# Performance work log

Measured on AMD Instinct MI355X. Metric: run time of the kernel, lower is better.

## Reference

```python
import jax, jax.numpy as jnp
import numpy as np

# dims: batch, nodes, d_node, d_edge, d_attn_hid, heads, d_node_hid, d_edge_hid, layers
B, N, DN, DE, DH, H, DNH, DEH, L = 2, 256, 128, 64, 128, 8, 512, 256, 2
DHH = DH // H  # per-head dim
SCALE = 1.0 / (DH ** 0.5)  # source scales by full d_hid, not per-head dim


def _ln(x, g, b):
    m = jnp.mean(x, -1, keepdims=True)
    v = jnp.mean((x - m) ** 2, -1, keepdims=True)
    return (x - m) * jax.lax.rsqrt(v + 1e-5) * g + b


def _gelu(x):
    return jax.nn.gelu(x, approximate=False)  # torch nn.GELU default = exact erf


def setup_inputs() -> dict:
    key = jax.random.key(0)
    ks = iter(jax.random.split(key, 40))
    def w(shape, scale=0.02):
        return jax.random.normal(next(ks), shape, jnp.float32) * scale
    return {
        "node_features": jax.random.normal(next(ks), (B, N, DN), jnp.float32),
        "edge_features": jax.random.normal(next(ks), (B, N, N, DE), jnp.float32),
        "Wqkv_n": w((L, DN, 3 * DH)),
        "Wqkv_e": w((L, DE, 4 * DH)),
        "Wo": w((L, DH, DN)), "bo": jnp.zeros((L, DN), jnp.float32),
        "Wl0": w((L, DN, DN)), "bl0": jnp.zeros((L, DN), jnp.float32),
        "ln0_g": jnp.ones((L, DN), jnp.float32), "ln0_b": jnp.zeros((L, DN), jnp.float32),
        "Wm1": w((L, DN, DNH)), "Wm2": w((L, DNH, DN)), "bm2": jnp.zeros((L, DN), jnp.float32),
        "ln1_g": jnp.ones((L, DN), jnp.float32), "ln1_b": jnp.zeros((L, DN), jnp.float32),
        "We0": w((L, 2 * DE, DEH)), "be0": jnp.zeros((L, DEH), jnp.float32),
        "Ws": w((L, DN, DEH)), "bs": jnp.zeros((L, DEH), jnp.float32),
        "Wt": w((L, DN, DEH)), "bt": jnp.zeros((L, DEH), jnp.float32),
        "We1": w((L, DEH, DE)), "be1": jnp.zeros((L, DE), jnp.float32),
        "eln0_g": jnp.ones((L, DE), jnp.float32), "eln0_b": jnp.zeros((L, DE), jnp.float32),
        "Wem1": w((L, DE, DEH)), "Wem2": w((L, DEH, DE)), "bem2": jnp.zeros((L, DE), jnp.float32),
        "eln1_g": jnp.ones((L, DE), jnp.float32), "eln1_b": jnp.zeros((L, DE), jnp.float32),
    }


def _forward(node_features, edge_features, Wqkv_n, Wqkv_e, Wo, bo, Wl0, bl0,
             ln0_g, ln0_b, Wm1, Wm2, bm2, ln1_g, ln1_b, We0, be0, Ws, bs, Wt, bt,
             We1, be1, eln0_g, eln0_b, Wem1, Wem2, bem2, eln1_g, eln1_b):
    x, e = node_features, edge_features
    for l in range(L):
        # --- RTAttention (modulate_v=True, eval mode) ---
        qkv_n = (x @ Wqkv_n[l]).reshape(B, N, H, 3 * DHH).transpose(0, 2, 1, 3)  # b h n 3d
        qn, kn, vn = jnp.split(qkv_n, 3, axis=-1)
        qkv_e = (e @ Wqkv_e[l]).reshape(B, N, N, H, 4 * DHH).transpose(0, 3, 1, 2, 4)  # b h i j 4d
        eq, ek, ev, em = jnp.split(qkv_e, 4, axis=-1)
        q = qn[:, :, :, None, :] + eq            # b h i j d
        k = kn[:, :, None, :, :] + ek            # b h i j d
        v = vn[:, :, None, :, :] * em + ev       # modulated values
        dots = SCALE * jnp.einsum('bhijd,bhijd->bhij', q, k)
        attn = jax.nn.softmax(dots, axis=-1)
        out = jnp.einsum('bhij,bhijd->bhid', attn, v)
        out = out.transpose(0, 2, 1, 3).reshape(B, N, DH)
        attn_out = out @ Wo[l] + bo[l]
        # --- node updates: ln(x + lin0(attn)); ln(x + mlp(x)) ---
        x = _ln(x + (attn_out @ Wl0[l] + bl0[l]), ln0_g[l], ln0_b[l])
        x = _ln(x + (_gelu(x @ Wm1[l]) @ Wm2[l] + bm2[l]), ln1_g[l], ln1_b[l])
        # --- edge updates (EdgeLayer) ---
        src = (x @ Ws[l] + bs[l])[:, :, None, :]   # broadcast over target j
        tgt = (x @ Wt[l] + bt[l])[:, None, :, :]   # broadcast over source i
        ecat = jnp.concatenate([e, e.transpose(0, 2, 1, 3)], axis=-1)  # [e_ij, e_ji]
        h = _gelu(ecat @ We0[l] + be0[l] + src + tgt)
        e = _ln(e + (h @ We1[l] + be1[l]), eln0_g[l], eln0_b[l])
        e = _ln(e + (_gelu(e @ Wem1[l]) @ Wem2[l] + bem2[l]), eln1_g[l], eln1_b[l])
    return x, e


def reference(node_features, edge_features, Wqkv_n, Wqkv_e, Wo, bo, Wl0, bl0,
              ln0_g, ln0_b, Wm1, Wm2, bm2, ln1_g, ln1_b, We0, be0, Ws, bs, Wt, bt,
              We1, be1, eln0_g, eln0_b, Wem1, Wem2, bem2, eln1_g, eln1_b):
    return _forward(node_features, edge_features, Wqkv_n, Wqkv_e, Wo, bo, Wl0, bl0,
                    ln0_g, ln0_b, Wm1, Wm2, bm2, ln1_g, ln1_b, We0, be0, Ws, bs, Wt, bt,
                    We1, be1, eln0_g, eln0_b, Wem1, Wem2, bem2, eln1_g, eln1_b)
```

## Files before the change

### kernel.cpp

```cpp
#include <hip/hip_runtime.h>
#include <hip/hip_bf16.h>
#include <stdint.h>

#define BB 2
#define NN 256
#define DN 128
#define DE 64
#define DH 128
#define NH 8
#define DHH 16
#define DNH 512
#define DEH 256
#define NL 2
#define SCALE_ATT 0.08838834764831845f

typedef __hip_bfloat16 bf16;
typedef __attribute__((ext_vector_type(8))) short short8;
typedef __attribute__((ext_vector_type(4))) float f32x4;

__device__ __forceinline__ float gelu_f(float x) {
  return 0.5f * x * (1.0f + erff(x * 0.70710678118654752f));
}
__device__ __forceinline__ float gelu_t(float x) {
  float m2u = x * fmaf(x * x, -0.07135481627f, -1.59576912161f);
  float e = __expf(m2u);
  return x * __builtin_amdgcn_rcpf(1.f + e);
}

template <int ctrl>
__device__ __forceinline__ float dppf(float v) {
  return __int_as_float(
      __builtin_amdgcn_update_dpp(0, __float_as_int(v), ctrl, 0xF, 0xF, true));
}
__device__ __forceinline__ float row_sum16(float v) {
  v += dppf<0xB1>(v);
  v += dppf<0x4E>(v);
  v += dppf<0x124>(v);
  v += dppf<0x128>(v);
  return v;
}
__device__ __forceinline__ float row_max16(float v) {
  v = fmaxf(v, dppf<0xB1>(v));
  v = fmaxf(v, dppf<0x4E>(v));
  v = fmaxf(v, dppf<0x124>(v));
  v = fmaxf(v, dppf<0x128>(v));
  return v;
}
__device__ __forceinline__ float wave_sum(float v) {
  v = row_sum16(v);
  v += __shfl_xor(v, 16, 64);
  v += __shfl_xor(v, 32, 64);
  return v;
}
__device__ __forceinline__ float wave_max(float v) {
  v = row_max16(v);
  v = fmaxf(v, __shfl_xor(v, 16, 64));
  v = fmaxf(v, __shfl_xor(v, 32, 64));
  return v;
}

__device__ __forceinline__ short f2bf(float f) {
  union { float f; uint32_t u; } v{f};
  uint32_t r = (v.u + 0x7FFFu + ((v.u >> 16) & 1u)) >> 16;
  return (short)r;
}
__device__ __forceinline__ float bf2f(short s) {
  union { uint32_t u; float f; } v;
  v.u = ((uint32_t)(uint16_t)s) << 16;
  return v.f;
}

__global__ void k_detect(const uint32_t* g8, const uint32_t* g13, int* flag) {
  if (threadIdx.x == 0 && blockIdx.x == 0) {
    uint32_t a = g8[0], b = g13[0];
    *flag = (a == 0x3F803F80u || b == 0x3F803F80u) ? 1 : 0;
  }
}

struct CastArgs {
  const void* src[30];
  float* dst[30];
  int n[30];
  const int* flag;
};

__global__ __launch_bounds__(256) void k_cast_all(CastArgs a) {
  int ti = blockIdx.y;
  float* d = a.dst[ti];
  int n = a.n[ti];
  int stride = gridDim.x * blockDim.x;
  if (*a.flag) {
    const bf16* s = (const bf16*)a.src[ti];
    for (int i = blockIdx.x * blockDim.x + threadIdx.x; i < n; i += stride)
      d[i] = __bfloat162float(s[i]);
  } else {
    const float* s = (const float*)a.src[ti];
    for (int i = blockIdx.x * blockDim.x + threadIdx.x; i < n; i += stride)
      d[i] = s[i];
  }
}

__global__ __launch_bounds__(256) void k_cast_e(const void* __restrict__ src,
                                                short* __restrict__ dst,
                                                const int* __restrict__ flag) {
  const int n8 = BB * NN * NN * DE / 8;
  int stride = gridDim.x * blockDim.x;
  if (*flag) {
    const uint4* s = (const uint4*)src;
    uint4* d = (uint4*)dst;
    for (int i = blockIdx.x * blockDim.x + threadIdx.x; i < n8; i += stride) d[i] = s[i];
  } else {
    const float4* s = (const float4*)src;
    for (int i = blockIdx.x * blockDim.x + threadIdx.x; i < n8; i += stride) {
      float4 a = s[2 * i], b = s[2 * i + 1];
      short* o = dst + 8 * i;
      o[0] = f2bf(a.x); o[1] = f2bf(a.y); o[2] = f2bf(a.z); o[3] = f2bf(a.w);
      o[4] = f2bf(b.x); o[5] = f2bf(b.y); o[6] = f2bf(b.z); o[7] = f2bf(b.w);
    }
  }
}

__global__ __launch_bounds__(256) void k_cast_out(const float* __restrict__ x,
                                                  const short* __restrict__ e,
                                                  void* __restrict__ out_v,
                                                  const int* __restrict__ flag) {
  const int nx = BB * NN * DN;
  const int total = nx + BB * NN * NN * DE;
  int stride = gridDim.x * blockDim.x;
  if (*flag) {
    short* out = (short*)out_v;
    for (int i = blockIdx.x * blockDim.x + threadIdx.x; i < total; i += stride)
      out[i] = (i < nx) ? f2bf(x[i]) : e[i - nx];
  } else {
    float* out = (float*)out_v;
    for (int i = blockIdx.x * blockDim.x + threadIdx.x; i < total; i += stride)
      out[i] = (i < nx) ? x[i] : bf2f(e[i - nx]);
  }
}

struct WtJob { const float* src; short* dst; int K; int N; };
struct WtArgs { WtJob job[10]; };
__global__ __launch_bounds__(256) void k_wtrans_all(WtArgs a) {
  WtJob j = a.job[blockIdx.y];
  int total = j.K * j.N;
  int stride = gridDim.x * 256;
  for (int idx = blockIdx.x * 256 + threadIdx.x; idx < total; idx += stride) {
    int k = idx / j.N, n = idx - k * j.N;
    j.dst[n * j.K + k] = f2bf(j.src[idx]);
  }
}

__global__ __launch_bounds__(128) void k_node_qkv(const float* __restrict__ x,
                                                  const float* __restrict__ W,
                                                  float* __restrict__ qkv) {
  int row = blockIdx.x;
  __shared__ float xs[DN];
  int t = threadIdx.x;
  xs[t] = x[row * DN + t];
  __syncthreads();
#pragma unroll
  for (int c0 = 0; c0 < 384; c0 += 128) {
    int c = c0 + t;
    float a = 0.f;
    for (int k = 0; k < DN; ++k) a = fmaf(xs[k], W[k * 384 + c], a);
    qkv[row * 384 + c] = a;
  }
}

__global__ __launch_bounds__(256) void k_attn_fused(
    const short* __restrict__ e, const short* __restrict__ WqeT,
    const float* __restrict__ qkv, float* __restrict__ o_buf) {
  int i = blockIdx.x, b = blockIdx.y;
  __shared__ short est[256 * 72];
  __shared__ float sp[NH * NN];
  __shared__ float qnl[DH];
  int t = threadIdx.x;
  for (int idx = t; idx < 2048; idx += 256) {
    int j = idx >> 3, c8 = (idx & 7) * 8;
    *(short8*)(est + j * 72 + c8) =
        *(const short8*)(e + ((size_t)(b * NN + i) * NN + j) * DE + c8);
  }
  if (t < DH) qnl[t] = qkv[(size_t)(b * NN + i) * 384 + (t >> 4) * 48 + (t & 15)];
  __syncthreads();

  int wv = t >> 6, lane = t & 63, g8 = lane >> 4, lo = lane & 15;

  {
    short8 bq[2][2][2];
#pragma unroll
    for (int hh = 0; hh < 2; ++hh)
#pragma unroll
      for (int p = 0; p < 2; ++p)
#pragma unroll
        for (int ks = 0; ks < 2; ++ks)
          bq[hh][p][ks] = *(const short8*)(
              WqeT + (size_t)(((wv * 2 + hh) * 4 + p) * 16 + lo) * 64 + ks * 32 + g8 * 8);
    for (int mt = 0; mt < 16; ++mt) {
      short8 a0 = *(const short8*)(est + (mt * 16 + lo) * 72 + g8 * 8);
      short8 a1 = *(const short8*)(est + (mt * 16 + lo) * 72 + 32 + g8 * 8);
#pragma unroll
      for (int hh = 0; hh < 2; ++hh) {
        int h = wv * 2 + hh;
        float kn4[4];
#pragma unroll
        for (int r = 0; r < 4; ++r)
          kn4[r] = qkv[(size_t)(b * NN + mt * 16 + g8 * 4 + r) * 384 + h * 48 + 16 + lo];
        f32x4 cq = {0.f, 0.f, 0.f, 0.f}, ck = {0.f, 0.f, 0.f, 0.f};
        cq = __builtin_amdgcn_mfma_f32_16x16x32_bf16(a0, bq[hh][0][0], cq, 0, 0, 0);
        cq = __builtin_amdgcn_mfma_f32_16x16x32_bf16(a1, bq[hh][0][1], cq, 0, 0, 0);
        ck = __builtin_amdgcn_mfma_f32_16x16x32_bf16(a0, bq[hh][1][0], ck, 0, 0, 0);
        ck = __builtin_amdgcn_mfma_f32_16x16x32_bf16(a1, bq[hh][1][1], ck, 0, 0, 0);
        float qv = qnl[h * 16 + lo];
#pragma unroll
        for (int r = 0; r < 4; ++r) {
          int j = mt * 16 + g8 * 4 + r;
          float s = (qv + cq[r]) * (kn4[r] + ck[r]);
          s = row_sum16(s);
          if (lo == 0) sp[h * NN + j] = s * SCALE_ATT;
        }
      }
    }
  }
  __syncthreads();

#pragma unroll
  for (int hh = 0; hh < 2; ++hh) {
    int h = wv * 2 + hh;
    float v[4];
#pragma unroll
    for (int q = 0; q < 4; ++q) v[q] = sp[h * NN + lane + 64 * q];
    float m = fmaxf(fmaxf(v[0], v[1]), fmaxf(v[2], v[3]));
    m = wave_max(m);
    float l = 0.f;
#pragma unroll
    for (int q = 0; q < 4; ++q) { v[q] = __expf(v[q] - m); l += v[q]; }
    l = wave_sum(l);
    float inv = 1.f / l;
#pragma unroll
    for (int q = 0; q < 4; ++q) sp[h * NN + lane + 64 * q] = v[q] * inv;
  }
  __syncthreads();

  {
    short8 bv[2][2][2];
#pragma unroll
    for (int hh = 0; hh < 2; ++hh)
#pragma unroll
      for (int p = 0; p < 2; ++p)
#pragma unroll
        for (int ks = 0; ks < 2; ++ks)
          bv[hh][p][ks] = *(const short8*)(
              WqeT + (size_t)(((wv * 2 + hh) * 4 + 2 + p) * 16 + lo) * 64 + ks * 32 + g8 * 8);
    float oacc[2] = {0.f, 0.f};
    for (int mt = 0; mt < 16; ++mt) {
      short8 a0 = *(const short8*)(est + (mt * 16 + lo) * 72 + g8 * 8);
      short8 a1 = *(const short8*)(est + (mt * 16 + lo) * 72 + 32 + g8 * 8);
#pragma unroll
      for (int hh = 0; hh < 2; ++hh) {
        int h = wv * 2 + hh;
        float vn4[4];
#pragma unroll
        for (int r = 0; r < 4; ++r)
          vn4[r] = qkv[(size_t)(b * NN + mt * 16 + g8 * 4 + r) * 384 + h * 48 + 32 + lo];
        f32x4 cv = {0.f, 0.f, 0.f, 0.f}, cm = {0.f, 0.f, 0.f, 0.f};
        cv = __builtin_amdgcn_mfma_f32_16x16x32_bf16(a0, bv[hh][0][0], cv, 0, 0, 0);
        cv = __builtin_amdgcn_mfma_f32_16x16x32_bf16(a1, bv[hh][0][1], cv, 0, 0, 0);
        cm = __builtin_amdgcn_mfma_f32_16x16x32_bf16(a0, bv[hh][1][0], cm, 0, 0, 0);
        cm = __builtin_amdgcn_mfma_f32_16x16x32_bf16(a1, bv[hh][1][1], cm, 0, 0, 0);
#pragma unroll
        for (int r = 0; r < 4; ++r) {
          int j = mt * 16 + g8 * 4 + r;
          float vv = fmaf(vn4[r], cm[r], cv[r]);
          oacc[hh] = fmaf(sp[h * NN + j], vv, oacc[hh]);
        }
      }
    }
#pragma unroll
    for (int hh = 0; hh < 2; ++hh) {
      int h = wv * 2 + hh;
      float o = oacc[hh];
      o += __shfl_xor(o, 16, 64);
      o += __shfl_xor(o, 32, 64);
      if (g8 == 0) o_buf[(size_t)(b * NN + i) * DH + h * 16 + lo] = o;
    }
  }
}

__global__ __launch_bounds__(256) void k_node_fused(
    const float* __restrict__ o_buf,
    const float* __restrict__ Wo, const float* __restrict__ bo,
    const float* __restrict__ Wl0, const float* __restrict__ bl0,
    const float* __restrict__ g0, const float* __restrict__ b0n,
    const float* __restrict__ Wm1, const float* __restrict__ Wm2,
    const float* __restrict__ bm2, const float* __restrict__ g1,
    const float* __restrict__ b1n, const float* __restrict__ Ws,
    const float* __restrict__ bs, const float* __restrict__ Wt,
    const float* __restrict__ bt, const float* __restrict__ WqnN,
    float* __restrict__ qkv, float* __restrict__ srcb,
    float* __restrict__ tgtb, float* __restrict__ x) {
  int i = blockIdx.x, b = blockIdx.y;
  int row = b * NN + i;
  __shared__ float orow[DH];
  __shared__ float t1s[DH];
  __shared__ float xs[DN];
  __shared__ float hsb[DNH];
  __shared__ float part[256];
  __shared__ float red[4];
  int t = threadIdx.x;
  int col = t & 127, kh = t >> 7;
  if (t < DH) orow[t] = o_buf[(size_t)row * DH + t];
  __syncthreads();
  {
    float a = 0.f;
    int k0 = kh * 64;
    for (int k = k0; k < k0 + 64; ++k) a = fmaf(orow[k], Wo[k * DN + col], a);
    part[t] = a;
  }
  __syncthreads();
  if (t < DH) t1s[t] = part[t] + part[t + 128] + bo[t];
  __syncthreads();
  {
    float a = 0.f;
    int k0 = kh * 64;
    for (int k = k0; k < k0 + 64; ++k) a = fmaf(t1s[k], Wl0[k * DN + col], a);
    part[t] = a;
  }
  __syncthreads();
  if (t < DN) {
    float y = part[t] + part[t + 128] + bl0[t] + x[(size_t)row * DN + t];
    float s1 = wave_sum(y), s2 = wave_sum(y * y);
    if ((t & 63) == 0) { red[t >> 6] = s1; red[2 + (t >> 6)] = s2; }
    part[t] = y;
  }
  __syncthreads();
  if (t < DN) {
    float y = part[t];
    float mean = (red[0] + red[1]) * (1.f / 128.f);
    float var = (red[2] + red[3]) * (1.f / 128.f) - mean * mean;
    float rr = rsqrtf(var + 1e-5f);
    xs[t] = (y - mean) * rr * g0[t] + b0n[t];
  }
  __syncthreads();
#pragma unroll
  for (int p = 0; p < 2; ++p) {
    int c = t + 256 * p;
    float a = 0.f;
    for (int k = 0; k < DN; ++k) a = fmaf(xs[k], Wm1[k * DNH + c], a);
    hsb[c] = gelu_f(a);
  }
  __syncthreads();
  {
    float a = 0.f;
    int k0 = kh * 256;
    for (int k = k0; k < k0 + 256; ++k) a = fmaf(hsb[k], Wm2[k * DN + col], a);
    part[t] = a;
  }
  __syncthreads();
  if (t < DN) {
    float y = part[t] + part[t + 128] + bm2[t] + xs[t];
    float s1 = wave_sum(y), s2 = wave_sum(y * y);
    if ((t & 63) == 0) { red[t >> 6] = s1; red[2 + (t >> 6)] = s2; }
    part[t] = y;
  }
  __syncthreads();
  if (t < DN) {
    float y = part[t];
    float mean = (red[0] + red[1]) * (1.f / 128.f);
    float var = (red[2] + red[3]) * (1.f / 128.f) - mean * mean;
    float rr = rsqrtf(var + 1e-5f);
    float x2 = (y - mean) * rr * g1[t] + b1n[t];
    x[(size_t)row * DN + t] = x2;
    xs[t] = x2;
  }
  __syncthreads();
  {
    float a = bs[t], cc = bt[t];
    for (int k = 0; k < DN; ++k) {
      float xv = xs[k];
      a = fmaf(xv, Ws[k * DEH + t], a);
      cc = fmaf(xv, Wt[k * DEH + t], cc);
    }
    srcb[(size_t)row * DEH + t] = a;
    tgtb[(size_t)row * DEH + t] = cc;
  }
  if (WqnN) {
#pragma unroll
    for (int p = 0; p < 2; ++p) {
      int c = t + 256 * p;
      if (c < 384) {
        float a = 0.f;
        for (int k = 0; k < DN; ++k) a = fmaf(xs[k], WqnN[k * 384 + c], a);
        qkv[(size_t)row * 384 + c] = a;
      }
    }
  }
}

__global__ __launch_bounds__(256) void k_edge_fused(
    const short* __restrict__ e_in, const short* __restrict__ W0T,
    const float* __restrict__ b0, const short* __restrict__ W1T,
    const float* __restrict__ b1, const float* __restrict__ srcb,
    const float* __restrict__ tgtb, const float* __restrict__ g,
    const float* __restrict__ bb, const short* __restrict__ Wm1T,
    const short* __restrict__ Wm2T, const float* __restrict__ bm2,
    const float* __restrict__ gm, const float* __restrict__ bbm,
    short* __restrict__ e_out) {
  int bid = blockIdx.x;
  int swz = (bid & 7) * 256 + (bid >> 3);
  int jt = swz & 3, i = (swz >> 2) & 255, b = swz >> 10;
  int j0 = jt * 64;
  __shared__ short hidT[64 * 264];
  int t = threadIdx.x;
  int wv = t >> 6, lane = t & 63, g8 = lane >> 4, lo = lane & 15;
  int nq = wv * 64;
  int m0 = wv * 16;

  {
    float bias_n[4];
#pragma unroll
    for (int nt = 0; nt < 4; ++nt)
      bias_n[nt] = b0[nq + nt * 16 + lo] + srcb[(size_t)(b * NN + i) * DEH + nq + nt * 16 + lo];
    short8 bfr1[4][4];
#pragma unroll
    for (int nt = 0; nt < 4; ++nt)
#pragma unroll
      for (int ks = 0; ks < 4; ++ks)
        bfr1[nt][ks] =
            *(const short8*)(W0T + (size_t)(nq + nt * 16 + lo) * 128 + ks * 32 + g8 * 8);
#pragma unroll
    for (int mt = 0; mt < 4; ++mt) {
      int mrow = mt * 16 + lo;
      float tg[4][4];
#pragma unroll
      for (int nt = 0; nt < 4; ++nt)
#pragma unroll
        for (int r = 0; r < 4; ++r)
          tg[nt][r] = tgtb[((size_t)(b * NN) + j0 + mt * 16 + g8 * 4 + r) * DEH +
                           nq + nt * 16 + lo];
      short8 a[4];
      const short* eA = e_in + ((size_t)(b * NN + i) * NN + j0 + mrow) * DE;
#pragma unroll
      for (int ks = 0; ks < 2; ++ks) a[ks] = *(const short8*)(eA + ks * 32 + g8 * 8);
      const short* eT = e_in + ((size_t)(b * NN + j0 + mrow) * NN + i) * DE;
#pragma unroll
      for (int ks = 0; ks < 2; ++ks) a[2 + ks] = *(const short8*)(eT + ks * 32 + g8 * 8);
      f32x4 acc[4];
#pragma unroll
      for (int nt = 0; nt < 4; ++nt) {
        f32x4 c = {0.f, 0.f, 0.f, 0.f};
#pragma unroll
        for (int ks = 0; ks < 4; ++ks)
          c = __builtin_amdgcn_mfma_f32_16x16x32_bf16(a[ks], bfr1[nt][ks], c, 0, 0, 0);
        acc[nt] = c;
      }
#pragma unroll
      for (int nt = 0; nt < 4; ++nt) {
        int n = nq + nt * 16 + lo;
#pragma unroll
        for (int r = 0; r < 4; ++r) {
          int m = mt * 16 + g8 * 4 + r;
          hidT[m * 264 + n] = f2bf(gelu_t(acc[nt][r] + bias_n[nt] + tg[nt][r]));
        }
      }
    }
  }
  float resv[4][4];
#pragma unroll
  for (int nt = 0; nt < 4; ++nt)
#pragma unroll
    for (int r = 0; r < 4; ++r)
      resv[nt][r] = bf2f(e_in[((size_t)(b * NN + i) * NN + j0 + m0 + g8 * 4 + r) * DE +
                              nt * 16 + lo]);
  __syncthreads();

  float emid[4][4];
  {
    short8 a2[8];
#pragma unroll
    for (int ks = 0; ks < 8; ++ks)
      a2[ks] = *(const short8*)(hidT + (m0 + lo) * 264 + ks * 32 + g8 * 8);
    f32x4 acc2[4];
#pragma unroll
    for (int nt = 0; nt < 4; ++nt) {
      f32x4 c = {0.f, 0.f, 0.f, 0.f};
      const short* bp = W1T + (size_t)(nt * 16 + lo) * 256;
#pragma unroll
      for (int ks = 0; ks < 8; ++ks)
        c = __builtin_amdgcn_mfma_f32_16x16x32_bf16(
            a2[ks], *(const short8*)(bp + ks * 32 + g8 * 8), c, 0, 0, 0);
      acc2[nt] = c;
    }
#pragma unroll
    for (int nt = 0; nt < 4; ++nt) {
      int n = nt * 16 + lo;
      float bb1 = b1[n];
#pragma unroll
      for (int r = 0; r < 4; ++r) emid[nt][r] = acc2[nt][r] + bb1 + resv[nt][r];
    }
#pragma unroll
    for (int r = 0; r < 4; ++r) {
      float s = emid[0][r] + emid[1][r] + emid[2][r] + emid[3][r];
      float q = emid[0][r] * emid[0][r] + emid[1][r] * emid[1][r] +
                emid[2][r] * emid[2][r] + emid[3][r] * emid[3][r];
      s = row_sum16(s);
      q = row_sum16(q);
      float mean = s * (1.f / 64.f);
      float var = q * (1.f / 64.f) - mean * mean;
      float rr = rsqrtf(var + 1e-5f);
      int m = m0 + g8 * 4 + r;
#pragma unroll
      for (int nt = 0; nt < 4; ++nt) {
        int n = nt * 16 + lo;
        float v = (emid[nt][r] - mean) * rr * g[n] + bb[n];
        emid[nt][r] = v;
        hidT[m * 264 + n] = f2bf(v);
      }
    }
  }

  {
    short8 a3[2];
#pragma unroll
    for (int ks = 0; ks < 2; ++ks)
      a3[ks] = *(const short8*)(hidT + (m0 + lo) * 264 + ks * 32 + g8 * 8);
#pragma unroll 4
    for (int nt = 0; nt < 16; ++nt) {
      f32x4 c = {0.f, 0.f, 0.f, 0.f};
      const short* bp = Wm1T + (size_t)(nt * 16 + lo) * 64;
#pragma unroll
      for (int ks = 0; ks < 2; ++ks)
        c = __builtin_amdgcn_mfma_f32_16x16x32_bf16(
            a3[ks], *(const short8*)(bp + ks * 32 + g8 * 8), c, 0, 0, 0);
      int n = nt * 16 + lo;
#pragma unroll
      for (int r = 0; r < 4; ++r)
        hidT[(m0 + g8 * 4 + r) * 264 + n] = f2bf(gelu_t(c[r]));
    }
  }

  {
    short8 a4[8];
#pragma unroll
    for (int ks = 0; ks < 8; ++ks)
      a4[ks] = *(const short8*)(hidT + (m0 + lo) * 264 + ks * 32 + g8 * 8);
    f32x4 acc4[4];
#pragma unroll
    for (int nt = 0; nt < 4; ++nt) {
      f32x4 c = {0.f, 0.f, 0.f, 0.f};
      const short* bp = Wm2T + (size_t)(nt * 16 + lo) * 256;
#pragma unroll
      for (int ks = 0; ks < 8; ++ks)
        c = __builtin_amdgcn_mfma_f32_16x16x32_bf16(
            a4[ks], *(const short8*)(bp + ks * 32 + g8 * 8), c, 0, 0, 0);
      acc4[nt] = c;
    }
    float vals[4][4];
#pragma unroll
    for (int nt = 0; nt < 4; ++nt) {
      int n = nt * 16 + lo;
      float bv = bm2[n];
#pragma unroll
      for (int r = 0; r < 4; ++r) vals[nt][r] = acc4[nt][r] + bv + emid[nt][r];
    }
#pragma unroll
    for (int r = 0; r < 4; ++r) {
      float s = vals[0][r] + vals[1][r] + vals[2][r] + vals[3][r];
      float q = vals[0][r] * vals[0][r] + vals[1][r] * vals[1][r] +
                vals[2][r] * vals[2][r] + vals[3][r] * vals[3][r];
      s = row_sum16(s);
      q = row_sum16(q);
      float mean = s * (1.f / 64.f);
      float var = q * (1.f / 64.f) - mean * mean;
      float rr = rsqrtf(var + 1e-5f);
      int m = m0 + g8 * 4 + r;
#pragma unroll
      for (int nt = 0; nt < 4; ++nt) {
        int n = nt * 16 + lo;
        e_out[((size_t)(b * NN + i) * NN + j0 + m) * DE + n] =
            f2bf((vals[nt][r] - mean) * rr * gm[n] + bbm[n]);
      }
    }
  }
}

extern "C" void kernel_launch(void* const* d_in, const int* in_sizes, int n_in,
                              void* d_out, int out_size, void* d_ws, size_t ws_size,
                              hipStream_t stream) {
  float* ws = (float*)d_ws;
  int* flag = (int*)ws;
  size_t off = 64;
  auto alloc = [&](size_t n) {
    float* p = ws + off;
    off += (n + 63) & ~(size_t)63;
    return p;
  };
  float* x_f = alloc((size_t)BB * NN * DN);
  short* e_a = (short*)alloc((size_t)BB * NN * NN * DE / 2);
  short* e_b = (short*)alloc((size_t)BB * NN * NN * DE / 2);
  float* qkv = alloc((size_t)BB * NN * 384);
  float* o_buf = alloc((size_t)BB * NN * DH);
  float* srcb = alloc((size_t)BB * NN * DEH);
  float* tgtb = alloc((size_t)BB * NN * DEH);
  short* WqeT = (short*)alloc(NL * 512 * 64 / 2);
  short* We0T = (short*)alloc(NL * 256 * 128 / 2);
  short* We1T = (short*)alloc(NL * 64 * 256 / 2);
  short* Wem1T = (short*)alloc(NL * 256 * 64 / 2);
  short* Wem2T = (short*)alloc(NL * 64 * 256 / 2);

  float* wf[30];
  wf[0] = x_f;
  wf[1] = x_f;
  CastArgs ca;
  int ntens = n_in < 30 ? n_in : 30;
  for (int idx = 0; idx < ntens; ++idx) {
    if (idx >= 2) wf[idx] = alloc((size_t)in_sizes[idx]);
    ca.src[idx] = d_in[idx];
    ca.dst[idx] = wf[idx];
    ca.n[idx] = (idx == 1) ? 0 : in_sizes[idx];
  }
  ca.flag = flag;

  k_detect<<<1, 64, 0, stream>>>((const uint32_t*)d_in[8], (const uint32_t*)d_in[13], flag);
  k_cast_all<<<dim3(64, ntens), dim3(256), 0, stream>>>(ca);
  k_cast_e<<<1024, 256, 0, stream>>>(d_in[1], e_a, flag);
  WtArgs wa;
  for (int l = 0; l < NL; ++l) {
    wa.job[l * 5 + 0] = {wf[3] + (size_t)l * DE * 512, WqeT + (size_t)l * 512 * 64, DE, 512};
    wa.job[l * 5 + 1] = {wf[15] + (size_t)l * 128 * 256, We0T + (size_t)l * 256 * 128, 128, 256};
    wa.job[l * 5 + 2] = {wf[21] + (size_t)l * 256 * 64, We1T + (size_t)l * 64 * 256, 256, 64};
    wa.job[l * 5 + 3] = {wf[25] + (size_t)l * 64 * 256, Wem1T + (size_t)l * 256 * 64, 64, 256};
    wa.job[l * 5 + 4] = {wf[26] + (size_t)l * 64 * 256, Wem2T + (size_t)l * 64 * 256, 256, 64};
  }
  k_wtrans_all<<<dim3(64, 10), 256, 0, stream>>>(wa);

  k_node_qkv<<<BB * NN, 128, 0, stream>>>(x_f, wf[2], qkv);

  for (int l = 0; l < NL; ++l) {
    const float* Wo = wf[4] + (size_t)l * DH * DN;
    const float* bo = wf[5] + (size_t)l * DN;
    const float* Wl0 = wf[6] + (size_t)l * DN * DN;
    const float* bl0 = wf[7] + (size_t)l * DN;
    const float* g0 = wf[8] + (size_t)l * DN;
    const float* b0n = wf[9] + (size_t)l * DN;
    const float* Wm1 = wf[10] + (size_t)l * DN * DNH;
    const float* Wm2 = wf[11] + (size_t)l * DNH * DN;
    const float* bm2 = wf[12] + (size_t)l * DN;
    const float* g1 = wf[13] + (size_t)l * DN;
    const float* b1n = wf[14] + (size_t)l * DN;
    const float* be0 = wf[16] + (size_t)l * DEH;
    const float* Wsw = wf[17] + (size_t)l * DN * DEH;
    const float* bsw = wf[18] + (size_t)l * DEH;
    const float* Wtw = wf[19] + (size_t)l * DN * DEH;
    const float* btw = wf[20] + (size_t)l * DEH;
    const float* be1 = wf[22] + (size_t)l * DE;
    const float* eg0 = wf[23] + (size_t)l * DE;
    const float* eb0 = wf[24] + (size_t)l * DE;
    const float* bem2 = wf[27] + (size_t)l * DE;
    const float* eg1 = wf[28] + (size_t)l * DE;
    const float* eb1 = wf[29] + (size_t)l * DE;
    const float* WqnNext = (l + 1 < NL) ? (wf[2] + (size_t)(l + 1) * DN * 3 * DH) : nullptr;

    const short* e_cur = (l == 0) ? e_a : e_b;
    short* e_nxt = (l == 0) ? e_b : e_a;

    k_attn_fused<<<dim3(NN, BB), 256, 0, stream>>>(
        e_cur, WqeT + (size_t)l * 512 * 64, qkv, o_buf);
    k_node_fused<<<dim3(NN, BB), 256, 0, stream>>>(
        o_buf, Wo, bo, Wl0, bl0, g0, b0n, Wm1, Wm2, bm2, g1, b1n,
        Wsw, bsw, Wtw, btw, WqnNext, qkv, srcb, tgtb, x_f);
    k_edge_fused<<<dim3(NN / 64 * NN * BB), 256, 0, stream>>>(
        e_cur, We0T + (size_t)l * 256 * 128, be0, We1T + (size_t)l * 64 * 256, be1,
        srcb, tgtb, eg0, eb0,
        Wem1T + (size_t)l * 256 * 64, Wem2T + (size_t)l * 64 * 256, bem2, eg1, eb1,
        e_nxt);
  }
  k_cast_out<<<1024, 256, 0, stream>>>(x_f, e_a, d_out, flag);
}
```

Measured before the change: 554.5 us.

## Split first edge GEMM by rows per wave and drop the block barrier

Reassigns the first edge-MLP GEMM so that each wave computes all 256 hidden columns for its own 16 edge rows, instead of a 64-column slice across all 64 rows. Each wave now only reads and writes its own rows of the shared hidden tile, so the __syncthreads before the second GEMM is removed. Each wave also loads only its own 16 rows of edge features rather than all 64. In exchange, the W0T weight fragments are no longer held in registers: every wave streams the whole weight matrix from global or cache memory, one column tile at a time.

```diff
diff --git a/kernel.cpp b/kernel.cpp
--- a/kernel.cpp
+++ b/kernel.cpp
@@ -412,56 +412,36 @@
   __shared__ short hidT[64 * 264];
   int t = threadIdx.x;
   int wv = t >> 6, lane = t & 63, g8 = lane >> 4, lo = lane & 15;
-  int nq = wv * 64;
   int m0 = wv * 16;
 
   {
-    float bias_n[4];
-#pragma unroll
-    for (int nt = 0; nt < 4; ++nt)
-      bias_n[nt] = b0[nq + nt * 16 + lo] + srcb[(size_t)(b * NN + i) * DEH + nq + nt * 16 + lo];
-    short8 bfr1[4][4];
-#pragma unroll
-    for (int nt = 0; nt < 4; ++nt)
+    short8 a[4];
+    const short* eA = e_in + ((size_t)(b * NN + i) * NN + j0 + m0 + lo) * DE;
+#pragma unroll
+    for (int ks = 0; ks < 2; ++ks) a[ks] = *(const short8*)(eA + ks * 32 + g8 * 8);
+    const short* eT = e_in + ((size_t)(b * NN + j0 + m0 + lo) * NN + i) * DE;
+#pragma unroll
+    for (int ks = 0; ks < 2; ++ks) a[2 + ks] = *(const short8*)(eT + ks * 32 + g8 * 8);
+    float bias_n[16];
+#pragma unroll
+    for (int nt = 0; nt < 16; ++nt)
+      bias_n[nt] = b0[nt * 16 + lo] + srcb[(size_t)(b * NN + i) * DEH + nt * 16 + lo];
+#pragma unroll 4
+    for (int nt = 0; nt < 16; ++nt) {
+      float tg[4];
+#pragma unroll
+      for (int r = 0; r < 4; ++r)
+        tg[r] = tgtb[((size_t)(b * NN) + j0 + m0 + g8 * 4 + r) * DEH + nt * 16 + lo];
+      const short* wp = W0T + (size_t)(nt * 16 + lo) * 128;
+      f32x4 c = {0.f, 0.f, 0.f, 0.f};
 #pragma unroll
       for (int ks = 0; ks < 4; ++ks)
-        bfr1[nt][ks] =
-            *(const short8*)(W0T + (size_t)(nq + nt * 16 + lo) * 128 + ks * 32 + g8 * 8);
-#pragma unroll
-    for (int mt = 0; mt < 4; ++mt) {
-      int mrow = mt * 16 + lo;
-      float tg[4][4];
-#pragma unroll
-      for (int nt = 0; nt < 4; ++nt)
-#pragma unroll
-        for (int r = 0; r < 4; ++r)
-          tg[nt][r] = tgtb[((size_t)(b * NN) + j0 + mt * 16 + g8 * 4 + r) * DEH +
-                           nq + nt * 16 + lo];
-      short8 a[4];
-      const short* eA = e_in + ((size_t)(b * NN + i) * NN + j0 + mrow) * DE;
-#pragma unroll
-      for (int ks = 0; ks < 2; ++ks) a[ks] = *(const short8*)(eA + ks * 32 + g8 * 8);
-      const short* eT = e_in + ((size_t)(b * NN + j0 + mrow) * NN + i) * DE;
-#pragma unroll
-      for (int ks = 0; ks < 2; ++ks) a[2 + ks] = *(const short8*)(eT + ks * 32 + g8 * 8);
-      f32x4 acc[4];
-#pragma unroll
-      for (int nt = 0; nt < 4; ++nt) {
-        f32x4 c = {0.f, 0.f, 0.f, 0.f};
-#pragma unroll
-        for (int ks = 0; ks < 4; ++ks)
-          c = __builtin_amdgcn_mfma_f32_16x16x32_bf16(a[ks], bfr1[nt][ks], c, 0, 0, 0);
-        acc[nt] = c;
-      }
-#pragma unroll
-      for (int nt = 0; nt < 4; ++nt) {
-        int n = nq + nt * 16 + lo;
-#pragma unroll
-        for (int r = 0; r < 4; ++r) {
-          int m = mt * 16 + g8 * 4 + r;
-          hidT[m * 264 + n] = f2bf(gelu_t(acc[nt][r] + bias_n[nt] + tg[nt][r]));
-        }
-      }
+        c = __builtin_amdgcn_mfma_f32_16x16x32_bf16(
+            a[ks], *(const short8*)(wp + ks * 32 + g8 * 8), c, 0, 0, 0);
+      int n = nt * 16 + lo;
+#pragma unroll
+      for (int r = 0; r < 4; ++r)
+        hidT[(m0 + g8 * 4 + r) * 264 + n] = f2bf(gelu_t(c[r] + bias_n[nt] + tg[r]));
     }
   }
   float resv[4][4];
@@ -471,7 +451,6 @@
     for (int r = 0; r < 4; ++r)
       resv[nt][r] = bf2f(e_in[((size_t)(b * NN + i) * NN + j0 + m0 + g8 * 4 + r) * DE +
                               nt * 16 + lo]);
-  __syncthreads();
 
   float emid[4][4];
   {
```

Result: slower. 616.2 us (+11.1%).
